# Performance work log

Hardware: AMD Instinct MI355X
Metric: run time of the kernel (lower is better)

The kernel has to match this reference:

```python
import jax, jax.numpy as jnp
import numpy as np

N, L, E_Q, E_TOTAL, H, FORECAST = 4, 2048, 512, 512, 8, 8
E_HEAD = E_TOTAL // H
DT = 1.0
NEG = -1e30


def setup_inputs() -> dict:
    rng = jax.random.key(0)
    ks = jax.random.split(rng, 8)
    inv = 1.0 / np.sqrt(E_Q)
    return {
        "query": jax.random.normal(ks[0], (N, L, E_Q), jnp.float32),
        "key": jax.random.normal(ks[1], (N, L, E_Q), jnp.float32),
        "value": jax.random.normal(ks[2], (N, L, E_Q), jnp.float32),
        "Wqkv": jax.random.normal(ks[3], (E_Q, 3 * E_TOTAL), jnp.float32) * inv,
        "bqkv": jnp.zeros((3 * E_TOTAL,), jnp.float32),
        "Wo": jax.random.normal(ks[4], (E_TOTAL, E_Q), jnp.float32) * (1.0 / np.sqrt(E_TOTAL)),
        "bo": jnp.zeros((E_Q,), jnp.float32),
        "Xi": jax.random.normal(ks[5], (H, E_HEAD, E_HEAD), jnp.float32) * 0.02,
    }


def reference(query, key, value, Wqkv, bqkv, Wo, bo, Xi):
    # NOTE: original forward projects `query` into q,k,v (key/value args unused).
    b, s, _ = query.shape
    qkv = query @ Wqkv + bqkv                      # [b, s, 3E]
    q, k, v = jnp.split(qkv, 3, axis=-1)
    split_heads = lambda t: t.reshape(b, s, H, E_HEAD).transpose(0, 2, 1, 3)  # [b,H,s,h]
    q, k, v = split_heads(q), split_heads(k), split_heads(v)
    # causal SDPA
    scale = 1.0 / np.sqrt(E_HEAD)
    scores = jnp.einsum('bhqd,bhkd->bhqk', q, k) * scale
    causal = jnp.tril(jnp.ones((s, s), bool))
    scores = jnp.where(causal, scores, NEG)
    probs = jax.nn.softmax(scores, axis=-1)
    attn = jnp.einsum('bhqk,bhkd->bhqd', probs, v)  # [b,H,s,h]
    # per-head SINDy linear dynamics, strict symmetry -> skew-symmetric A
    A = Xi - jnp.swapaxes(Xi, -1, -2)               # [H,h,h]

    def step(x, _):
        x2 = x + DT * jnp.einsum('bhsd,hde->bhse', x, A)
        return x2, x2

    _, ys = jax.lax.scan(step, attn, None, length=FORECAST)  # [n,b,H,s,h]
    roll = jnp.transpose(ys, (1, 0, 3, 2, 4)).reshape(b, FORECAST, s, E_TOTAL)
    return roll @ Wo + bo                            # [b, n, s, E_q]
```

## Files before the change

kernel.cpp:

```cpp
#include <hip/hip_runtime.h>
#include <math.h>


#define NEGV -1e30f

typedef __bf16 bf16_t;
typedef __bf16 bf16x4 __attribute__((ext_vector_type(4)));
typedef __bf16 bf16x8 __attribute__((ext_vector_type(8)));
typedef float f32x4 __attribute__((ext_vector_type(4)));

#define MFMA(a, b, c) __builtin_amdgcn_mfma_f32_16x16x32_bf16((a), (b), (c), 0, 0, 0)

#define QSCALE 0.18033688011112042f

__device__ __forceinline__ bf16x8* swz_ptr(bf16_t* base, int r, int cb) {
  return (bf16x8*)((char*)base + r * 128 + (cb ^ ((r & 7) << 4)));
}
__device__ __forceinline__ const bf16x8* swz_cptr(const bf16_t* base, int r, int cb) {
  return (const bf16x8*)((const char*)base + r * 128 + (cb ^ ((r & 7) << 4)));
}

__device__ __forceinline__ void gload16(const bf16_t* g, bf16_t* l) {
  __builtin_amdgcn_global_load_lds(
      (const __attribute__((address_space(1))) void*)g,
      (__attribute__((address_space(3))) void*)l, 16, 0, 0);
}


__global__ __launch_bounds__(256) void xconv(const float* __restrict__ X,
                                             bf16_t* __restrict__ Xb) {
  const int gid = blockIdx.x * 256 + threadIdx.x;
  const int s = gid >> 6, j = gid & 63;
  const float4* src = (const float4*)(X + (size_t)s * 512 + j * 8);
  const float4 f0 = src[0], f1 = src[1];
  bf16x8 v;
  v[0] = (bf16_t)f0.x; v[1] = (bf16_t)f0.y; v[2] = (bf16_t)f0.z; v[3] = (bf16_t)f0.w;
  v[4] = (bf16_t)f1.x; v[5] = (bf16_t)f1.y; v[6] = (bf16_t)f1.z; v[7] = (bf16_t)f1.w;
  *(bf16x8*)&Xb[(size_t)s * 512 + (j >> 3) * 64 + 8 * ((j & 7) ^ (s & 7))] = v;
}

__global__ __launch_bounds__(256) void wconv(const float* __restrict__ W,
                                             bf16_t* __restrict__ WT) {
  const int n0 = blockIdx.x * 64, k0 = blockIdx.y * 64;
  __shared__ float Wf[64][65];
  const int tid = threadIdx.x;
#pragma unroll
  for (int c = 0; c < 16; ++c) {
    const int idx = tid + c * 256;
    const int kk = idx >> 6, nn = idx & 63;
    Wf[kk][nn] = W[(size_t)(k0 + kk) * 1536 + n0 + nn];
  }
  __syncthreads();
  const int nr = tid >> 2;
  const int jb = (tid & 3) * 2;
#pragma unroll
  for (int t = 0; t < 2; ++t) {
    const int j = jb + t;
    bf16x8 v;
#pragma unroll
    for (int i = 0; i < 8; ++i) v[i] = (bf16_t)Wf[j * 8 + i][nr];
    *(bf16x8*)&WT[(size_t)(n0 + nr) * 512 + k0 + 8 * (j ^ (nr & 7))] = v;
  }
}

__global__ __launch_bounds__(256) void build_powers(const float* __restrict__ Xi,
                                                    float* __restrict__ pows) {
  const int h = blockIdx.x;
  __shared__ __align__(16) float P[64][68];
  __shared__ __align__(16) float cur[64][68];
  const int tid = threadIdx.x;
  const float* xi = Xi + (size_t)h * 4096;
  float* dst = pows + (size_t)h * 8 * 4096;
  for (int idx = tid; idx < 4096; idx += 256) {
    const int i = idx >> 6, j = idx & 63;
    const float p = (i == j ? 1.f : 0.f) + xi[i * 64 + j] - xi[j * 64 + i];
    P[i][j] = p;
    cur[i][j] = p;
    dst[idx] = p;
  }
  __syncthreads();
  const int i = tid >> 2;
  const int j0 = (tid & 3) * 16;
  for (int n = 1; n < 8; ++n) {
    float a[16];
#pragma unroll
    for (int jj = 0; jj < 16; ++jj) a[jj] = 0.f;
    for (int dd = 0; dd < 64; ++dd) {
      const float c = cur[i][dd];
#pragma unroll
      for (int jj = 0; jj < 16; ++jj) a[jj] += c * P[dd][j0 + jj];
    }
    __syncthreads();
#pragma unroll
    for (int jj = 0; jj < 16; ++jj) {
      cur[i][j0 + jj] = a[jj];
      dst[n * 4096 + i * 64 + j0 + jj] = a[jj];
    }
    __syncthreads();
  }
}

__global__ __launch_bounds__(256) void build_B(const float* __restrict__ pows,
                                               const float* __restrict__ Wo,
                                               bf16_t* __restrict__ BmatT) {
  const int et = blockIdx.x;
  const int n = blockIdx.y;
  const int h = blockIdx.z;
  __shared__ __align__(16) float P[64][68];
  __shared__ __align__(16) float We[64][128];
  const int tid = threadIdx.x;
  const float* src = pows + ((size_t)h * 8 + n) * 4096;
  for (int idx = tid; idx < 4096; idx += 256) P[idx >> 6][idx & 63] = src[idx];
  const int e0 = et * 128;
  for (int idx = tid; idx < 8192; idx += 256) {
    const int dd = idx >> 7, e = idx & 127;
    We[dd][e] = Wo[(size_t)(h * 64 + dd) * 512 + e0 + e];
  }
  __syncthreads();
  const int d = tid >> 2;
  const int eq = (tid & 3) * 32;
  float acc[32];
#pragma unroll
  for (int j = 0; j < 32; ++j) acc[j] = 0.f;
  for (int dd = 0; dd < 64; ++dd) {
    const float p = P[d][dd];
#pragma unroll
    for (int j = 0; j < 32; ++j) acc[j] += p * We[dd][eq + j];
  }
  bf16_t* dst = BmatT + (size_t)n * 512 * 512 + (size_t)(e0 + eq) * 512 + h * 64;
  const int dlo = d & 7, dhi = d >> 3;
#pragma unroll
  for (int j = 0; j < 32; ++j)
    dst[(size_t)j * 512 + 8 * (dhi ^ (j & 7)) + dlo] = (bf16_t)acc[j];
}

__global__ __launch_bounds__(256) void qkv_gemm(const bf16_t* __restrict__ Xb,
                                                const bf16_t* __restrict__ WT,
                                                const float* __restrict__ bias,
                                                bf16_t* __restrict__ qw,
                                                bf16_t* __restrict__ kw,
                                                bf16_t* __restrict__ vt) {
  __shared__ __align__(16) bf16_t As[2][128 * 64];
  __shared__ __align__(16) bf16_t Bs[2][128 * 64];
  const int tid = threadIdx.x;
  const int wave = tid >> 6, lane = tid & 63;
  const int g = lane >> 4, li = lane & 15;
  const int row0 = blockIdx.x * 128;
  const int col0 = blockIdx.y * 128;
  const int wm = (wave >> 1) * 64, wn = (wave & 1) * 64;
  f32x4 acc[4][4] = {};
  const bf16_t* asrc = Xb + (size_t)(row0 + wave * 32 + (lane >> 3)) * 512 + (lane & 7) * 8;
  const bf16_t* bsrc = WT + (size_t)(col0 + wave * 32 + (lane >> 3)) * 512 + (lane & 7) * 8;
  bf16_t* adst0 = &As[0][wave * 32 * 64];
  bf16_t* adst1 = &As[1][wave * 32 * 64];
  bf16_t* bdst0 = &Bs[0][wave * 32 * 64];
  bf16_t* bdst1 = &Bs[1][wave * 32 * 64];
  auto stage = [&](int bi, int kt) {
    const int k0 = kt * 64;
    bf16_t* ad = bi ? adst1 : adst0;
    bf16_t* bd = bi ? bdst1 : bdst0;
#pragma unroll
    for (int c = 0; c < 4; ++c) {
      gload16(asrc + (size_t)c * 8 * 512 + k0, ad + c * 512);
      gload16(bsrc + (size_t)c * 8 * 512 + k0, bd + c * 512);
    }
  };
  stage(0, 0);
#pragma unroll
  for (int t = 0; t < 8; ++t) {
    const int cur = t & 1;
    if (t < 7) {
      stage(cur ^ 1, t + 1);
      asm volatile("s_waitcnt vmcnt(8)" ::: "memory");
    } else {
      asm volatile("s_waitcnt vmcnt(0)" ::: "memory");
    }
    __builtin_amdgcn_s_barrier();
    __builtin_amdgcn_sched_barrier(0);
#pragma unroll
    for (int ks = 0; ks < 2; ++ks) {
      bf16x8 af[4], bfr[4];
#pragma unroll
      for (int mr = 0; mr < 4; ++mr)
        af[mr] = *swz_cptr(As[cur], wm + mr * 16 + li, ks * 64 + g * 16);
#pragma unroll
      for (int nr = 0; nr < 4; ++nr)
        bfr[nr] = *swz_cptr(Bs[cur], wn + nr * 16 + li, ks * 64 + g * 16);
#pragma unroll
      for (int mr = 0; mr < 4; ++mr)
#pragma unroll
        for (int nr = 0; nr < 4; ++nr)
          acc[mr][nr] = MFMA(af[mr], bfr[nr], acc[mr][nr]);
    }
    __builtin_amdgcn_s_barrier();
    __builtin_amdgcn_sched_barrier(0);
  }
  const int cbase = col0 + wn;
  const int sel = cbase >> 9;
  const int hh = (cbase & 511) >> 6;
  const int bb = row0 >> 11;
  const size_t hb = (size_t)(bb * 8 + hh) * (2048 * 64);
  if (sel == 2) {
    bf16_t* vbase = vt + hb;
#pragma unroll
    for (int nr = 0; nr < 4; ++nr) {
      const int dcol = nr * 16 + li;
      const float bv = bias[cbase + dcol];
#pragma unroll
      for (int mr = 0; mr < 4; ++mr) {
        bf16x4 pk;
#pragma unroll
        for (int i = 0; i < 4; ++i) pk[i] = (bf16_t)(acc[mr][nr][i] + bv);
        const int s = (row0 + wm + mr * 16 + g * 4) & 2047;
        *(bf16x4*)&vbase[(size_t)dcol * 2048 + s] = pk;
      }
    }
  } else {
    bf16_t* dstp = (sel == 0 ? qw : kw) + hb;
    const float sc = (sel == 0) ? QSCALE : 1.0f;
#pragma unroll
    for (int nr = 0; nr < 4; ++nr) {
      const int dcol = nr * 16 + li;
      const float bv = bias[cbase + dcol];
#pragma unroll
      for (int mr = 0; mr < 4; ++mr) {
#pragma unroll
        for (int i = 0; i < 4; ++i) {
          const int r = row0 + wm + mr * 16 + g * 4 + i;
          const int s = r & 2047;
          dstp[(size_t)s * 64 + dcol] = (bf16_t)((acc[mr][nr][i] + bv) * sc);
        }
      }
    }
  }
}

__global__ __launch_bounds__(256) void fattn(const bf16_t* __restrict__ qw,
                                             const bf16_t* __restrict__ kw,
                                             const bf16_t* __restrict__ vt,
                                             bf16_t* __restrict__ attn,
                                             float* __restrict__ opart,
                                             float* __restrict__ ml) {
  __shared__ __align__(16) bf16_t Ks[2][64][64];
  __shared__ __align__(16) bf16_t Vs[2][64][64];
  __shared__ __align__(16) bf16_t Ps[4][16][64];
  const int tid = threadIdx.x;
  const int w = tid >> 6;
  const int lane = tid & 63;
  const int g = lane >> 4;
  const int li = lane & 15;
  const int x = blockIdx.x;
  int qt, ktb, kte, chunk;
  bool split;
  if (x < 16) {
    qt = 31 - x; ktb = 0; kte = 16; chunk = 0; split = true;
  } else if (x < 32) {
    qt = 47 - x; ktb = 16; kte = qt + 1; chunk = 1; split = true;
  } else {
    qt = 47 - x; ktb = 0; kte = qt + 1; chunk = 0; split = false;
  }
  const int h = blockIdx.y;
  const int b = blockIdx.z;
  const size_t base = ((size_t)(b * 8 + h)) * (2048 * 64);
  const int q0 = qt * 64;
  const int qrow = q0 + w * 16 + li;
  const bf16x8 aq0 = *(const bf16x8*)(qw + base + (size_t)qrow * 64 + g * 8);
  const bf16x8 aq1 = *(const bf16x8*)(qw + base + (size_t)qrow * 64 + 32 + g * 8);
  const bf16_t* kbase = kw + base;
  const bf16_t* vbase = vt + base;
  const int r_st = tid >> 2;
  const int qu = tid & 3;
  {
    const bf16_t* kp = kbase + (size_t)(ktb * 64 + r_st) * 64 + qu * 16;
    const bf16_t* vp = vbase + (size_t)r_st * 2048 + ktb * 64 + qu * 16;
    *swz_ptr(&Ks[0][0][0], r_st, qu * 32) = *(const bf16x8*)kp;
    *swz_ptr(&Ks[0][0][0], r_st, qu * 32 + 16) = *(const bf16x8*)(kp + 8);
    *swz_ptr(&Vs[0][0][0], r_st, qu * 32) = *(const bf16x8*)vp;
    *swz_ptr(&Vs[0][0][0], r_st, qu * 32 + 16) = *(const bf16x8*)(vp + 8);
  }
  f32x4 accO[4] = {};
  float m_run = -__builtin_inff();
  float l_run = 0.f;
  char* const psrow = (char*)&Ps[w][li][0];
  const int pswz = (li & 7) << 4;
  for (int kt = ktb; kt < kte; ++kt) {
    __syncthreads();
    const int cur = (kt - ktb) & 1;
    const bool pf = (kt + 1) < kte;
    bf16x8 nk0, nk1, nv0, nv1;
    if (pf) {
      const int kb2 = (kt + 1) * 64;
      const bf16_t* kp = kbase + (size_t)(kb2 + r_st) * 64 + qu * 16;
      const bf16_t* vp = vbase + (size_t)r_st * 2048 + kb2 + qu * 16;
      nk0 = *(const bf16x8*)kp;
      nk1 = *(const bf16x8*)(kp + 8);
      nv0 = *(const bf16x8*)vp;
      nv1 = *(const bf16x8*)(vp + 8);
    }
    f32x4 sv[4];
    __builtin_amdgcn_s_setprio(1);
#pragma unroll
    for (int nt = 0; nt < 4; ++nt) {
      const bf16x8 bk0 = *swz_cptr(&Ks[cur][0][0], nt * 16 + li, g * 16);
      const bf16x8 bk1 = *swz_cptr(&Ks[cur][0][0], nt * 16 + li, 64 + g * 16);
      f32x4 z = {0.f, 0.f, 0.f, 0.f};
      z = MFMA(bk0, aq0, z);
      sv[nt] = MFMA(bk1, aq1, z);
    }
    __builtin_amdgcn_s_setprio(0);
    if (kt == qt) {
#pragma unroll
      for (int nt = 0; nt < 4; ++nt)
#pragma unroll
        for (int i = 0; i < 4; ++i)
          if (nt * 16 + g * 4 + i > w * 16 + li) sv[nt][i] = NEGV;
    }
    float pmax = sv[0][0];
#pragma unroll
    for (int nt = 0; nt < 4; ++nt)
#pragma unroll
      for (int i = 0; i < 4; ++i) pmax = fmaxf(pmax, sv[nt][i]);
    pmax = fmaxf(pmax, __shfl_xor(pmax, 16, 64));
    pmax = fmaxf(pmax, __shfl_xor(pmax, 32, 64));
    if (!__all(pmax - m_run <= 8.f)) {
      const float newm = fmaxf(m_run, pmax);
      const float sc = exp2f(m_run - newm);
      l_run *= sc;
      m_run = newm;
#pragma unroll
      for (int nt = 0; nt < 4; ++nt)
#pragma unroll
        for (int i = 0; i < 4; ++i) accO[nt][i] *= sc;
    }
    float rsum = 0.f;
#pragma unroll
    for (int nt = 0; nt < 4; ++nt) {
#pragma unroll
      for (int i = 0; i < 4; ++i) {
        const float p = exp2f(sv[nt][i] - m_run);
        sv[nt][i] = p;
        rsum += p;
      }
    }
    rsum += __shfl_xor(rsum, 16, 64);
    rsum += __shfl_xor(rsum, 32, 64);
    l_run += rsum;
#pragma unroll
    for (int nt = 0; nt < 4; ++nt) {
      bf16x4 pk;
#pragma unroll
      for (int i = 0; i < 4; ++i) pk[i] = (bf16_t)sv[nt][i];
      *(bf16x4*)(psrow + ((nt * 32 + g * 8) ^ pswz)) = pk;
    }
    const bf16x8 ap0 = *(const bf16x8*)(psrow + ((g * 16) ^ pswz));
    const bf16x8 ap1 = *(const bf16x8*)(psrow + ((64 + g * 16) ^ pswz));
    __builtin_amdgcn_s_setprio(1);
#pragma unroll
    for (int nt = 0; nt < 4; ++nt) {
      const bf16x8 bv0 = *swz_cptr(&Vs[cur][0][0], nt * 16 + li, g * 16);
      const bf16x8 bv1 = *swz_cptr(&Vs[cur][0][0], nt * 16 + li, 64 + g * 16);
      accO[nt] = MFMA(bv0, ap0, accO[nt]);
      accO[nt] = MFMA(bv1, ap1, accO[nt]);
    }
    __builtin_amdgcn_s_setprio(0);
    if (pf) {
      *swz_ptr(&Ks[cur ^ 1][0][0], r_st, qu * 32) = nk0;
      *swz_ptr(&Ks[cur ^ 1][0][0], r_st, qu * 32 + 16) = nk1;
      *swz_ptr(&Vs[cur ^ 1][0][0], r_st, qu * 32) = nv0;
      *swz_ptr(&Vs[cur ^ 1][0][0], r_st, qu * 32 + 16) = nv1;
    }
  }
  if (!split) {
    const float inv = 1.0f / l_run;
    bf16_t* arow = attn + (size_t)(b * 2048 + qrow) * 512 + h * 64;
#pragma unroll
    for (int nt = 0; nt < 4; ++nt) {
      bf16x4 pk;
#pragma unroll
      for (int i = 0; i < 4; ++i) pk[i] = (bf16_t)(accO[nt][i] * inv);
      *(bf16x4*)&arow[8 * ((nt * 2 + (g >> 1)) ^ (li & 7)) + (g & 1) * 4] = pk;
    }
  } else {
    const int row = w * 16 + li;
    const size_t pbase = (((size_t)(b * 8 + h) * 16 + (qt - 16)) * 2 + chunk) * 64 + row;
    float* op = opart + pbase * 64;
#pragma unroll
    for (int nt = 0; nt < 4; ++nt) *(f32x4*)&op[nt * 16 + g * 4] = accO[nt];
    if (g == 0) {
      ml[pbase * 2] = m_run;
      ml[pbase * 2 + 1] = l_run;
    }
  }
}

__global__ __launch_bounds__(256) void fcombine(const float* __restrict__ opart,
                                                const float* __restrict__ ml,
                                                bf16_t* __restrict__ attn) {
  const int qi = blockIdx.x;
  const int h = blockIdx.y;
  const int b = blockIdx.z;
  const int tid = threadIdx.x;
  const int row = tid >> 2;
  const int dq = (tid & 3) * 16;
  const size_t base2 = ((size_t)(b * 8 + h) * 16 + qi) * 2;
  const size_t p0 = (base2 * 64 + row);
  const size_t p1 = ((base2 + 1) * 64 + row);
  const float m1 = ml[p0 * 2], l1 = ml[p0 * 2 + 1];
  const float m2 = ml[p1 * 2], l2 = ml[p1 * 2 + 1];
  const float m = fmaxf(m1, m2);
  const float w1 = exp2f(m1 - m), w2 = exp2f(m2 - m);
  const float inv = 1.0f / (l1 * w1 + l2 * w2);
  const float* o1 = opart + p0 * 64;
  const float* o2 = opart + p1 * 64;
  const int qrow = (16 + qi) * 64 + row;
  bf16_t* arow = attn + (size_t)(b * 2048 + qrow) * 512 + h * 64;
#pragma unroll
  for (int t = 0; t < 2; ++t) {
    const int c0 = dq + t * 8;
    const f32x4 a1 = *(const f32x4*)&o1[c0];
    const f32x4 b1 = *(const f32x4*)&o1[c0 + 4];
    const f32x4 a2 = *(const f32x4*)&o2[c0];
    const f32x4 b2 = *(const f32x4*)&o2[c0 + 4];
    bf16x8 v;
#pragma unroll
    for (int i = 0; i < 4; ++i) {
      v[i] = (bf16_t)((a1[i] * w1 + a2[i] * w2) * inv);
      v[4 + i] = (bf16_t)((b1[i] * w1 + b2[i] * w2) * inv);
    }
    *(bf16x8*)&arow[8 * ((c0 >> 3) ^ (row & 7))] = v;
  }
}

__global__ __launch_bounds__(256) void out_gemm(const bf16_t* __restrict__ A,
                                                const bf16_t* __restrict__ BmatT,
                                                const float* __restrict__ bo,
                                                float* __restrict__ out) {
  __shared__ __align__(16) bf16_t As[2][128 * 64];
  __shared__ __align__(16) bf16_t Bs[2][128 * 64];
  const int tid = threadIdx.x;
  const int wave = tid >> 6, lane = tid & 63;
  const int g = lane >> 4, li = lane & 15;
  const int row0 = blockIdx.x * 128;
  const int col0 = blockIdx.y * 128;
  const int nf = blockIdx.z;
  const int wm = (wave >> 1) * 64, wn = (wave & 1) * 64;
  f32x4 acc[4][4] = {};
  const bf16_t* asrc = A + (size_t)(row0 + wave * 32 + (lane >> 3)) * 512 + (lane & 7) * 8;
  const bf16_t* bsrc = BmatT + (size_t)nf * 512 * 512 +
                       (size_t)(col0 + wave * 32 + (lane >> 3)) * 512 + (lane & 7) * 8;
  bf16_t* adst0 = &As[0][wave * 32 * 64];
  bf16_t* adst1 = &As[1][wave * 32 * 64];
  bf16_t* bdst0 = &Bs[0][wave * 32 * 64];
  bf16_t* bdst1 = &Bs[1][wave * 32 * 64];
  auto stage = [&](int bi, int kt) {
    const int k0 = kt * 64;
    bf16_t* ad = bi ? adst1 : adst0;
    bf16_t* bd = bi ? bdst1 : bdst0;
#pragma unroll
    for (int c = 0; c < 4; ++c) {
      gload16(asrc + (size_t)c * 8 * 512 + k0, ad + c * 512);
      gload16(bsrc + (size_t)c * 8 * 512 + k0, bd + c * 512);
    }
  };
  stage(0, 0);
#pragma unroll
  for (int t = 0; t < 8; ++t) {
    const int cur = t & 1;
    if (t < 7) {
      stage(cur ^ 1, t + 1);
      asm volatile("s_waitcnt vmcnt(8)" ::: "memory");
    } else {
      asm volatile("s_waitcnt vmcnt(0)" ::: "memory");
    }
    __builtin_amdgcn_s_barrier();
    __builtin_amdgcn_sched_barrier(0);
#pragma unroll
    for (int ks = 0; ks < 2; ++ks) {
      bf16x8 af[4], bfr[4];
#pragma unroll
      for (int mr = 0; mr < 4; ++mr)
        af[mr] = *swz_cptr(As[cur], wm + mr * 16 + li, ks * 64 + g * 16);
#pragma unroll
      for (int nr = 0; nr < 4; ++nr)
        bfr[nr] = *swz_cptr(Bs[cur], wn + nr * 16 + li, ks * 64 + g * 16);
#pragma unroll
      for (int mr = 0; mr < 4; ++mr)
#pragma unroll
        for (int nr = 0; nr < 4; ++nr)
          acc[mr][nr] = MFMA(af[mr], bfr[nr], acc[mr][nr]);
    }
    __builtin_amdgcn_s_barrier();
    __builtin_amdgcn_sched_barrier(0);
  }
  const int bb = row0 >> 11;
  float* obase = out + ((size_t)(bb * 8 + nf)) * (2048 * 512);
#pragma unroll
  for (int nr = 0; nr < 4; ++nr) {
    const int c = col0 + wn + nr * 16 + li;
    const float bv = bo[c];
#pragma unroll
    for (int mr = 0; mr < 4; ++mr) {
#pragma unroll
      for (int i = 0; i < 4; ++i) {
        const int r = row0 + wm + mr * 16 + g * 4 + i;
        const int s = r & 2047;
        obase[(size_t)s * 512 + c] = acc[mr][nr][i] + bv;
      }
    }
  }
}

extern "C" void kernel_launch(void* const* d_in, const int* in_sizes, int n_in,
                              void* d_out, int out_size, void* d_ws, size_t ws_size,
                              hipStream_t stream) {
  const float* query = (const float*)d_in[0];
  const float* Wqkv = (const float*)d_in[3];
  const float* bqkv = (const float*)d_in[4];
  const float* Wo = (const float*)d_in[5];
  const float* bo = (const float*)d_in[6];
  const float* Xi = (const float*)d_in[7];
  float* out = (float*)d_out;

  char* ws = (char*)d_ws;
  bf16_t* qw = (bf16_t*)(ws + 0);
  bf16_t* kw = (bf16_t*)(ws + 8388608);
  bf16_t* vt = (bf16_t*)(ws + 16777216);
  bf16_t* Xb = (bf16_t*)(ws + 25165824);
  bf16_t* attn = (bf16_t*)(ws + 25165824);
  bf16_t* BmatT = (bf16_t*)(ws + 33554432);
  float* pows = (float*)(ws + 37748736);
  bf16_t* WT = (bf16_t*)(ws + 38797312);
  float* opart = (float*)(ws + 40370176);
  float* mlbuf = (float*)(ws + 57147392);

  xconv<<<dim3(2048), dim3(256), 0, stream>>>(query, Xb);
  wconv<<<dim3(24, 8), dim3(256), 0, stream>>>(Wqkv, WT);
  build_powers<<<dim3(8), dim3(256), 0, stream>>>(Xi, pows);
  build_B<<<dim3(4, 8, 8), dim3(256), 0, stream>>>(pows, Wo, BmatT);
  qkv_gemm<<<dim3(64, 12), dim3(256), 0, stream>>>(Xb, WT, bqkv, qw, kw, vt);
  fattn<<<dim3(48, 8, 4), dim3(256), 0, stream>>>(qw, kw, vt, attn, opart, mlbuf);
  fcombine<<<dim3(16, 8, 4), dim3(256), 0, stream>>>(opart, mlbuf, attn);
  out_gemm<<<dim3(64, 4, 8), dim3(256), 0, stream>>>(attn, BmatT, bo, out);
}
```

Baseline: 183.7 us.

## Fuse prep kernels into one launch and move P operand through cross-lane permutes

```diff
diff --git a/kernel.cpp b/kernel.cpp
--- a/kernel.cpp
+++ b/kernel.cpp
@@ -8,6 +8,7 @@
 typedef __bf16 bf16x4 __attribute__((ext_vector_type(4)));
 typedef __bf16 bf16x8 __attribute__((ext_vector_type(8)));
 typedef float f32x4 __attribute__((ext_vector_type(4)));
+typedef unsigned u32x4 __attribute__((ext_vector_type(4)));
 
 #define MFMA(a, b, c) __builtin_amdgcn_mfma_f32_16x16x32_bf16((a), (b), (c), 0, 0, 0)
 
@@ -26,77 +27,85 @@
       (__attribute__((address_space(3))) void*)l, 16, 0, 0);
 }
 
-
-__global__ __launch_bounds__(256) void xconv(const float* __restrict__ X,
-                                             bf16_t* __restrict__ Xb) {
-  const int gid = blockIdx.x * 256 + threadIdx.x;
-  const int s = gid >> 6, j = gid & 63;
-  const float4* src = (const float4*)(X + (size_t)s * 512 + j * 8);
-  const float4 f0 = src[0], f1 = src[1];
-  bf16x8 v;
-  v[0] = (bf16_t)f0.x; v[1] = (bf16_t)f0.y; v[2] = (bf16_t)f0.z; v[3] = (bf16_t)f0.w;
-  v[4] = (bf16_t)f1.x; v[5] = (bf16_t)f1.y; v[6] = (bf16_t)f1.z; v[7] = (bf16_t)f1.w;
-  *(bf16x8*)&Xb[(size_t)s * 512 + (j >> 3) * 64 + 8 * ((j & 7) ^ (s & 7))] = v;
-}
-
-__global__ __launch_bounds__(256) void wconv(const float* __restrict__ W,
-                                             bf16_t* __restrict__ WT) {
-  const int n0 = blockIdx.x * 64, k0 = blockIdx.y * 64;
-  __shared__ float Wf[64][65];
+__device__ __forceinline__ unsigned cvt_pk_bf16(float lo, float hi) {
+  unsigned r;
+  asm("v_cvt_pk_bf16_f32 %0, %1, %2" : "=v"(r) : "v"(lo), "v"(hi));
+  return r;
+}
+
+
+__global__ __launch_bounds__(256) void prep(const float* __restrict__ X,
+                                            const float* __restrict__ W,
+                                            const float* __restrict__ Xi,
+                                            bf16_t* __restrict__ Xb,
+                                            bf16_t* __restrict__ WT,
+                                            float* __restrict__ pows) {
+  __shared__ __align__(16) char smem[2 * 64 * 68 * 4];
+  const int bx = blockIdx.x;
   const int tid = threadIdx.x;
-#pragma unroll
-  for (int c = 0; c < 16; ++c) {
-    const int idx = tid + c * 256;
-    const int kk = idx >> 6, nn = idx & 63;
-    Wf[kk][nn] = W[(size_t)(k0 + kk) * 1536 + n0 + nn];
-  }
-  __syncthreads();
-  const int nr = tid >> 2;
-  const int jb = (tid & 3) * 2;
-#pragma unroll
-  for (int t = 0; t < 2; ++t) {
-    const int j = jb + t;
+  if (bx < 8) {
+    const int h = bx;
+    float (*P)[68] = (float(*)[68])smem;
+    float (*cur)[68] = (float(*)[68])(smem + 64 * 68 * 4);
+    const float* xi = Xi + (size_t)h * 4096;
+    float* dst = pows + (size_t)h * 8 * 4096;
+    for (int idx = tid; idx < 4096; idx += 256) {
+      const int i = idx >> 6, j = idx & 63;
+      const float p = (i == j ? 1.f : 0.f) + xi[i * 64 + j] - xi[j * 64 + i];
+      P[i][j] = p;
+      cur[i][j] = p;
+      dst[idx] = p;
+    }
+    __syncthreads();
+    const int i = tid >> 2;
+    const int j0 = (tid & 3) * 16;
+    for (int n = 1; n < 8; ++n) {
+      float a[16];
+#pragma unroll
+      for (int jj = 0; jj < 16; ++jj) a[jj] = 0.f;
+      for (int dd = 0; dd < 64; ++dd) {
+        const float c = cur[i][dd];
+#pragma unroll
+        for (int jj = 0; jj < 16; ++jj) a[jj] += c * P[dd][j0 + jj];
+      }
+      __syncthreads();
+#pragma unroll
+      for (int jj = 0; jj < 16; ++jj) {
+        cur[i][j0 + jj] = a[jj];
+        dst[n * 4096 + i * 64 + j0 + jj] = a[jj];
+      }
+      __syncthreads();
+    }
+  } else if (bx < 200) {
+    const int idx = bx - 8;
+    const int n0 = (idx % 24) * 64, k0 = (idx / 24) * 64;
+    float (*Wf)[65] = (float(*)[65])smem;
+#pragma unroll
+    for (int c = 0; c < 16; ++c) {
+      const int id2 = tid + c * 256;
+      const int kk = id2 >> 6, nn = id2 & 63;
+      Wf[kk][nn] = W[(size_t)(k0 + kk) * 1536 + n0 + nn];
+    }
+    __syncthreads();
+    const int nr = tid >> 2;
+    const int jb = (tid & 3) * 2;
+#pragma unroll
+    for (int t = 0; t < 2; ++t) {
+      const int j = jb + t;
+      bf16x8 v;
+#pragma unroll
+      for (int i = 0; i < 8; ++i) v[i] = (bf16_t)Wf[j * 8 + i][nr];
+      *(bf16x8*)&WT[(size_t)(n0 + nr) * 512 + k0 + 8 * (j ^ (nr & 7))] = v;
+    }
+  } else {
+    const int gid = (bx - 200) * 256 + tid;
+    const int s = gid >> 6, j = gid & 63;
+    const float4* src = (const float4*)(X + (size_t)s * 512 + j * 8);
+    const float4 f0 = src[0], f1 = src[1];
     bf16x8 v;
-#pragma unroll
-    for (int i = 0; i < 8; ++i) v[i] = (bf16_t)Wf[j * 8 + i][nr];
-    *(bf16x8*)&WT[(size_t)(n0 + nr) * 512 + k0 + 8 * (j ^ (nr & 7))] = v;
-  }
-}
-
-__global__ __launch_bounds__(256) void build_powers(const float* __restrict__ Xi,
-                                                    float* __restrict__ pows) {
-  const int h = blockIdx.x;
-  __shared__ __align__(16) float P[64][68];
-  __shared__ __align__(16) float cur[64][68];
-  const int tid = threadIdx.x;
-  const float* xi = Xi + (size_t)h * 4096;
-  float* dst = pows + (size_t)h * 8 * 4096;
-  for (int idx = tid; idx < 4096; idx += 256) {
-    const int i = idx >> 6, j = idx & 63;
-    const float p = (i == j ? 1.f : 0.f) + xi[i * 64 + j] - xi[j * 64 + i];
-    P[i][j] = p;
-    cur[i][j] = p;
-    dst[idx] = p;
-  }
-  __syncthreads();
-  const int i = tid >> 2;
-  const int j0 = (tid & 3) * 16;
-  for (int n = 1; n < 8; ++n) {
-    float a[16];
-#pragma unroll
-    for (int jj = 0; jj < 16; ++jj) a[jj] = 0.f;
-    for (int dd = 0; dd < 64; ++dd) {
-      const float c = cur[i][dd];
-#pragma unroll
-      for (int jj = 0; jj < 16; ++jj) a[jj] += c * P[dd][j0 + jj];
-    }
-    __syncthreads();
-#pragma unroll
-    for (int jj = 0; jj < 16; ++jj) {
-      cur[i][j0 + jj] = a[jj];
-      dst[n * 4096 + i * 64 + j0 + jj] = a[jj];
-    }
-    __syncthreads();
+    v[0] = (bf16_t)f0.x; v[1] = (bf16_t)f0.y; v[2] = (bf16_t)f0.z; v[3] = (bf16_t)f0.w;
+    v[4] = (bf16_t)f1.x; v[5] = (bf16_t)f1.y; v[6] = (bf16_t)f1.z; v[7] = (bf16_t)f1.w;
+    *(bf16x8*)&Xb[(size_t)s * 512 + (j >> 3) * 64 + 8 * ((j & 7) ^ (s & 7))] = v;
   }
 }
 
@@ -243,7 +252,6 @@
                                              float* __restrict__ ml) {
   __shared__ __align__(16) bf16_t Ks[2][64][64];
   __shared__ __align__(16) bf16_t Vs[2][64][64];
-  __shared__ __align__(16) bf16_t Ps[4][16][64];
   const int tid = threadIdx.x;
   const int w = tid >> 6;
   const int lane = tid & 63;
@@ -281,8 +289,6 @@
   f32x4 accO[4] = {};
   float m_run = -__builtin_inff();
   float l_run = 0.f;
-  char* const psrow = (char*)&Ps[w][li][0];
-  const int pswz = (li & 7) << 4;
   for (int kt = ktb; kt < kte; ++kt) {
     __syncthreads();
     const int cur = (kt - ktb) & 1;
@@ -345,15 +351,31 @@
     rsum += __shfl_xor(rsum, 16, 64);
     rsum += __shfl_xor(rsum, 32, 64);
     l_run += rsum;
-#pragma unroll
-    for (int nt = 0; nt < 4; ++nt) {
-      bf16x4 pk;
-#pragma unroll
-      for (int i = 0; i < 4; ++i) pk[i] = (bf16_t)sv[nt][i];
-      *(bf16x4*)(psrow + ((nt * 32 + g * 8) ^ pswz)) = pk;
-    }
-    const bf16x8 ap0 = *(const bf16x8*)(psrow + ((g * 16) ^ pswz));
-    const bf16x8 ap1 = *(const bf16x8*)(psrow + ((64 + g * 16) ^ pswz));
+    const unsigned pk00 = cvt_pk_bf16(sv[0][0], sv[0][1]);
+    const unsigned pk01 = cvt_pk_bf16(sv[0][2], sv[0][3]);
+    const unsigned pk10 = cvt_pk_bf16(sv[1][0], sv[1][1]);
+    const unsigned pk11 = cvt_pk_bf16(sv[1][2], sv[1][3]);
+    const unsigned pk20 = cvt_pk_bf16(sv[2][0], sv[2][1]);
+    const unsigned pk21 = cvt_pk_bf16(sv[2][2], sv[2][3]);
+    const unsigned pk30 = cvt_pk_bf16(sv[3][0], sv[3][1]);
+    const unsigned pk31 = cvt_pk_bf16(sv[3][2], sv[3][3]);
+    bf16x8 ap0, ap1;
+    {
+      auto s0 = __builtin_amdgcn_permlane32_swap((int)pk00, (int)pk10, false, false);
+      auto t0 = __builtin_amdgcn_permlane16_swap(s0[0], s0[1], false, false);
+      auto s1 = __builtin_amdgcn_permlane32_swap((int)pk01, (int)pk11, false, false);
+      auto t1 = __builtin_amdgcn_permlane16_swap(s1[0], s1[1], false, false);
+      u32x4 wd = {(unsigned)t0[0], (unsigned)t1[0], (unsigned)t0[1], (unsigned)t1[1]};
+      ap0 = __builtin_bit_cast(bf16x8, wd);
+    }
+    {
+      auto s0 = __builtin_amdgcn_permlane32_swap((int)pk20, (int)pk30, false, false);
+      auto t0 = __builtin_amdgcn_permlane16_swap(s0[0], s0[1], false, false);
+      auto s1 = __builtin_amdgcn_permlane32_swap((int)pk21, (int)pk31, false, false);
+      auto t1 = __builtin_amdgcn_permlane16_swap(s1[0], s1[1], false, false);
+      u32x4 wd = {(unsigned)t0[0], (unsigned)t1[0], (unsigned)t0[1], (unsigned)t1[1]};
+      ap1 = __builtin_bit_cast(bf16x8, wd);
+    }
     __builtin_amdgcn_s_setprio(1);
 #pragma unroll
     for (int nt = 0; nt < 4; ++nt) {
@@ -533,9 +555,7 @@
   float* opart = (float*)(ws + 40370176);
   float* mlbuf = (float*)(ws + 57147392);
 
-  xconv<<<dim3(2048), dim3(256), 0, stream>>>(query, Xb);
-  wconv<<<dim3(24, 8), dim3(256), 0, stream>>>(Wqkv, WT);
-  build_powers<<<dim3(8), dim3(256), 0, stream>>>(Xi, pows);
+  prep<<<dim3(2248), dim3(256), 0, stream>>>(query, Wqkv, Xi, Xb, WT, pows);
   build_B<<<dim3(4, 8, 8), dim3(256), 0, stream>>>(pows, Wo, BmatT);
   qkv_gemm<<<dim3(64, 12), dim3(256), 0, stream>>>(Xb, WT, bqkv, qw, kw, vt);
   fattn<<<dim3(48, 8, 4), dim3(256), 0, stream>>>(qw, kw, vt, attn, opart, mlbuf);
```

Result: faster. 179.4 us (median of 2 runs) (-2.3%).
